# Performance work log

Measured on AMD Instinct MI355X. Metric: run time of the kernel, lower is better.

The kernel has to match this reference:

```python
import jax, jax.numpy as jnp
import numpy as np

C = 512
C8 = C // 8  # 64
B, H, W = 4, 64, 64


def setup_inputs() -> dict:
    key = jax.random.key(0)
    ks = jax.random.split(key, 8)
    s_in = 1.0 / np.sqrt(C)
    return {
        "x": jax.random.normal(ks[0], (B, C, H, W), dtype=jnp.float32),
        "Wf": jax.random.normal(ks[1], (C8, C), dtype=jnp.float32) * s_in,
        "bf": jax.random.normal(ks[2], (C8,), dtype=jnp.float32) * 0.01,
        "Wg": jax.random.normal(ks[3], (C8, C), dtype=jnp.float32) * s_in,
        "bg": jax.random.normal(ks[4], (C8,), dtype=jnp.float32) * 0.01,
        "Wh": jax.random.normal(ks[5], (C, C), dtype=jnp.float32) * s_in,
        "bh": jax.random.normal(ks[6], (C,), dtype=jnp.float32) * 0.01,
        # original inits gamma=0; use small nonzero so the attention path is exercised
        "gamma": jax.random.normal(ks[7], (1,), dtype=jnp.float32) * 0.1,
    }


def reference(x, Wf, bf, Wg, bg, Wh, bh, gamma):
    b, c, h, w = x.shape
    n = h * w
    xt = x.reshape(b, c, n)  # flatten spatial -> tokens (b, C, N)
    # 1x1 convs are per-token GEMMs
    f = jnp.einsum('bcn,oc->bno', xt, Wf) + bf          # (b, N, C8)
    g = jnp.einsum('bcn,oc->bon', xt, Wg) + bg[:, None]  # (b, C8, N)
    attn = jax.nn.softmax(jnp.einsum('bnk,bkm->bnm', f, g), axis=2)  # (b, N, N)
    hv = jnp.einsum('bcn,oc->bon', xt, Wh) + bh[:, None]  # (b, C, N)
    # torch.bmm(h, attention): out[:,c,j] = sum_i h[:,c,i] * attn[:,i,j]
    sa = jnp.einsum('bci,bij->bcj', hv, attn).reshape(b, c, h, w)
    return gamma[0] * sa + x
```

## Files before the change

kernel.cpp:

```cpp
#include <hip/hip_runtime.h>


#define Bq 4
#define Cq 512
#define Nq 4096
#define PSTR 72

typedef __attribute__((ext_vector_type(8))) short bf16x8;
typedef __attribute__((ext_vector_type(4))) float f32x4;

__device__ __forceinline__ short f2bf(float f) {
  unsigned u = __float_as_uint(f);
  u += 0x7fffu + ((u >> 16) & 1u);
  return (short)(u >> 16);
}
__device__ __forceinline__ float bf2f(short h) {
  return __uint_as_float(((unsigned)(unsigned short)h) << 16);
}

#define MFMA16(A, B, C) __builtin_amdgcn_mfma_f32_16x16x32_bf16((A), (B), (C), 0, 0, 0)

__device__ __forceinline__ size_t fg_frag(int b, int t16, int ss) {
  return ((size_t)((b * 256 + t16) * 2 + ss)) * 512;
}
__device__ __forceinline__ size_t hv_frag(int b, int tc, int si) {
  return ((size_t)((b * 32 + tc) * 128 + si)) * 512;
}

__global__ __launch_bounds__(256) void k_prepw(
    const float* __restrict__ Wf, const float* __restrict__ Wg,
    const float* __restrict__ Wh,
    short* __restrict__ whi, short* __restrict__ wlo, short* __restrict__ whb) {
  int gid = blockIdx.x * 256 + threadIdx.x;
  if (gid < 128 * 512) {
    int row = gid >> 9;
    float v = (row < 64) ? Wf[gid] : Wg[gid - 32768];
    short h = f2bf(v);
    whi[gid] = h;
    wlo[gid] = f2bf(v - bf2f(h));
  }
  whb[gid] = f2bf(Wh[gid]);
}

__global__ __launch_bounds__(256) void k_xpose(
    const float* __restrict__ x, short* __restrict__ xthi, short* __restrict__ xtlo) {
  int b = blockIdx.z, c0 = blockIdx.y * 64, n0 = blockIdx.x * 64;
  __shared__ float tile[64][65];
  int t = threadIdx.x;
  int l = t & 15, g = t >> 4;
  const float* xp = x + ((size_t)b * Cq + c0) * Nq + n0;
#pragma unroll
  for (int e = 0; e < 4; e++) {
    int cl = g + e * 16;
    float4 v = *(const float4*)(xp + (size_t)cl * Nq + l * 4);
    tile[cl][l * 4 + 0] = v.x; tile[cl][l * 4 + 1] = v.y;
    tile[cl][l * 4 + 2] = v.z; tile[cl][l * 4 + 3] = v.w;
  }
  __syncthreads();
#pragma unroll
  for (int e = 0; e < 4; e++) {
    int nl = g + e * 16;
    short hi[4], lo[4];
#pragma unroll
    for (int qq = 0; qq < 4; qq++) {
      float v = tile[l * 4 + qq][nl];
      hi[qq] = f2bf(v);
      lo[qq] = f2bf(v - bf2f(hi[qq]));
    }
    size_t off = ((size_t)b * Nq + n0 + nl) * Cq + c0 + l * 4;
    *(short4*)(xthi + off) = make_short4(hi[0], hi[1], hi[2], hi[3]);
    *(short4*)(xtlo + off) = make_short4(lo[0], lo[1], lo[2], lo[3]);
  }
}

__global__ __launch_bounds__(512) void k_fg(
    const short* __restrict__ xthi, const short* __restrict__ xtlo,
    const short* __restrict__ whi, const short* __restrict__ wlo,
    const float* __restrict__ bfv, const float* __restrict__ bgv,
    short* __restrict__ ffh, short* __restrict__ ffl,
    short* __restrict__ gfh, short* __restrict__ gfl) {
  int b = blockIdx.y, n0 = blockIdx.x * 64;
  int t = threadIdx.x, w = t >> 6, lane = t & 63, l15 = lane & 15, q = lane >> 4;
  int wr = w & 3, wh = w >> 2;
  const short* ah = xthi + ((size_t)b * Nq + n0 + wr * 16 + l15) * Cq;
  const short* al = xtlo + ((size_t)b * Nq + n0 + wr * 16 + l15) * Cq;
  f32x4 z = {0.f, 0.f, 0.f, 0.f};
  f32x4 acc[4] = {z, z, z, z};
  for (int ks = 0; ks < 16; ks++) {
    bf16x8 Ahi = *(const bf16x8*)(ah + ks * 32 + q * 8);
    bf16x8 Alo = *(const bf16x8*)(al + ks * 32 + q * 8);
#pragma unroll
    for (int os = 0; os < 4; os++) {
      int o = wh * 64 + os * 16 + l15;
      bf16x8 Bhi = *(const bf16x8*)(whi + o * 512 + ks * 32 + q * 8);
      bf16x8 Blo = *(const bf16x8*)(wlo + o * 512 + ks * 32 + q * 8);
      acc[os] = MFMA16(Alo, Bhi, acc[os]);
      acc[os] = MFMA16(Ahi, Blo, acc[os]);
      acc[os] = MFMA16(Ahi, Bhi, acc[os]);
    }
  }
#pragma unroll
  for (int os = 0; os < 4; os++) {
#pragma unroll
    for (int r = 0; r < 4; r++) {
      int o = os * 16 + l15;
      int n = n0 + wr * 16 + q * 4 + r;
      float v = acc[os][r] + (wh == 0 ? bfv[o] : bgv[o]);
      size_t off = ((size_t)((b * 256 + (n >> 4)) * 2 + (o >> 5))) * 512
                 + (((o >> 3) & 3) * 16 + (n & 15)) * 8 + (o & 7);
      short h = f2bf(v);
      short lo = f2bf(v - bf2f(h));
      if (wh == 0) { ffh[off] = h; ffl[off] = lo; }
      else         { gfh[off] = h; gfl[off] = lo; }
    }
  }
}

__global__ __launch_bounds__(512) void k_stats(
    const short* __restrict__ ffh, const short* __restrict__ ffl,
    const short* __restrict__ gfh, const short* __restrict__ gfl,
    float* __restrict__ lsum4) {
  int jch = blockIdx.x, jc = jch * 1024, i0 = blockIdx.y * 64, b = blockIdx.z;
  int t = threadIdx.x, w = t >> 6, lane = t & 63, l15 = lane & 15, q = lane >> 4;
  bf16x8 Ahi[4][2], Alo[4][2];
#pragma unroll
  for (int ig = 0; ig < 4; ig++)
#pragma unroll
    for (int ss = 0; ss < 2; ss++) {
      size_t base = fg_frag(b, (i0 >> 4) + ig, ss) + lane * 8;
      Ahi[ig][ss] = *(const bf16x8*)(ffh + base);
      Alo[ig][ss] = *(const bf16x8*)(ffl + base);
    }
  float ls[16];
#pragma unroll
  for (int a = 0; a < 16; a++) ls[a] = 0.f;
  f32x4 z = {0.f, 0.f, 0.f, 0.f};
  for (int jt = 0; jt < 8; jt++) {
    int tj = (jc >> 4) + w * 8 + jt;
    bf16x8 GBh[2], GBl[2];
#pragma unroll
    for (int ss = 0; ss < 2; ss++) {
      size_t base = fg_frag(b, tj, ss) + lane * 8;
      GBh[ss] = *(const bf16x8*)(gfh + base);
      GBl[ss] = *(const bf16x8*)(gfl + base);
    }
#pragma unroll
    for (int ig = 0; ig < 4; ig++) {
      f32x4 sh = z, sl = z;
#pragma unroll
      for (int ss = 0; ss < 2; ss++) {
        sl = MFMA16(Alo[ig][ss], GBh[ss], sl);
        sl = MFMA16(Ahi[ig][ss], GBl[ss], sl);
        sh = MFMA16(Ahi[ig][ss], GBh[ss], sh);
      }
#pragma unroll
      for (int r = 0; r < 4; r++) ls[ig * 4 + r] += __expf(sh[r] + sl[r]);
    }
  }
#pragma unroll
  for (int m = 1; m < 16; m <<= 1) {
#pragma unroll
    for (int a = 0; a < 16; a++) ls[a] += __shfl_xor(ls[a], m, 64);
  }
  __shared__ float part[8][64];
  if (l15 == 0) {
#pragma unroll
    for (int ig = 0; ig < 4; ig++)
#pragma unroll
      for (int r = 0; r < 4; r++) part[w][ig * 16 + q * 4 + r] = ls[ig * 4 + r];
  }
  __syncthreads();
  if (t < 64) {
    float s = 0.f;
#pragma unroll
    for (int ww = 0; ww < 8; ww++) s += part[ww][t];
    lsum4[(size_t)jch * 16384 + (size_t)b * Nq + i0 + t] = s;
  }
}

__global__ __launch_bounds__(512) void k_hv(
    const short* __restrict__ whb, const short* __restrict__ xthi,
    const float* __restrict__ bhv, const float* __restrict__ lsum4,
    short* __restrict__ hvf) {
  int si = blockIdx.x, b = blockIdx.y;
  int t = threadIdx.x, w = t >> 6, lane = t & 63, l15 = lane & 15, q = lane >> 4;
  int c0 = w * 64;
  const short* ar0 = xthi + ((size_t)b * Nq + si * 32 + l15) * Cq;
  const short* ar1 = ar0 + 16 * Cq;
  f32x4 z = {0.f, 0.f, 0.f, 0.f};
  f32x4 acc[2][4];
#pragma unroll
  for (int a = 0; a < 2; a++)
#pragma unroll
    for (int c = 0; c < 4; c++) acc[a][c] = z;
  for (int ks = 0; ks < 16; ks++) {
    bf16x8 A0 = *(const bf16x8*)(ar0 + ks * 32 + q * 8);
    bf16x8 A1 = *(const bf16x8*)(ar1 + ks * 32 + q * 8);
#pragma unroll
    for (int ct = 0; ct < 4; ct++) {
      bf16x8 Bv = *(const bf16x8*)(whb + (size_t)(c0 + ct * 16 + l15) * 512 + ks * 32 + q * 8);
      acc[0][ct] = MFMA16(A0, Bv, acc[0][ct]);
      acc[1][ct] = MFMA16(A1, Bv, acc[1][ct]);
    }
  }
  float li[2][4];
#pragma unroll
  for (int it = 0; it < 2; it++)
#pragma unroll
    for (int r = 0; r < 4; r++) {
      size_t idx = (size_t)b * Nq + si * 32 + it * 16 + q * 4 + r;
      float s = lsum4[idx] + lsum4[16384 + idx] + lsum4[32768 + idx] + lsum4[49152 + idx];
      li[it][r] = 1.0f / s;
    }
  int src0 = ((q & 1) << 5) + l15;
  int src1 = src0 + 16;
  int hiSel = q >> 1;
#pragma unroll
  for (int ct = 0; ct < 4; ct++) {
    float bias = bhv[c0 + ct * 16 + l15];
    unsigned u01[2], u23[2];
#pragma unroll
    for (int it = 0; it < 2; it++) {
      float v0 = (acc[it][ct][0] + bias) * li[it][0];
      float v1 = (acc[it][ct][1] + bias) * li[it][1];
      float v2 = (acc[it][ct][2] + bias) * li[it][2];
      float v3 = (acc[it][ct][3] + bias) * li[it][3];
      u01[it] = (unsigned)(unsigned short)f2bf(v0) | ((unsigned)(unsigned short)f2bf(v1) << 16);
      u23[it] = (unsigned)(unsigned short)f2bf(v2) | ((unsigned)(unsigned short)f2bf(v3) << 16);
    }
    unsigned a0 = __shfl((int)u01[0], src0), b0 = __shfl((int)u01[1], src0);
    unsigned a1 = __shfl((int)u23[0], src0), b1 = __shfl((int)u23[1], src0);
    unsigned a2 = __shfl((int)u01[0], src1), b2 = __shfl((int)u01[1], src1);
    unsigned a3 = __shfl((int)u23[0], src1), b3 = __shfl((int)u23[1], src1);
    uint4 st;
    st.x = hiSel ? b0 : a0;
    st.y = hiSel ? b1 : a1;
    st.z = hiSel ? b2 : a2;
    st.w = hiSel ? b3 : a3;
    *(uint4*)(hvf + hv_frag(b, (c0 >> 4) + ct, si) + (size_t)lane * 8) = st;
  }
}

__global__ __launch_bounds__(1024, 4) void k_attn(
    const short* __restrict__ ffh, const short* __restrict__ ffl,
    const short* __restrict__ gfh, const short* __restrict__ gfl,
    const short* __restrict__ hvf, const float* __restrict__ x,
    const float* __restrict__ gp, float* __restrict__ out) {
  int L = blockIdx.x;
  int b = (L & 7) >> 1;
  int jt64 = ((L >> 3) << 1) | (L & 1);
  int j0 = jt64 * 64;
  int t = threadIdx.x, w = t >> 6, lane = t & 63, l15 = lane & 15, q = lane >> 4;
  int iq = w & 3, jh = w >> 2;
  int cg = w & 7, jg = w >> 3;
  __shared__ __align__(16) short pt[2][64 * PSTR];
  float gamma = gp[0];
  f32x4 z = {0.f, 0.f, 0.f, 0.f};
  f32x4 acc[4][2];
#pragma unroll
  for (int a = 0; a < 4; a++)
#pragma unroll
    for (int bb = 0; bb < 2; bb++) acc[a][bb] = z;
  bf16x8 GBh[2], GBl[2];
#pragma unroll
  for (int ss = 0; ss < 2; ss++) {
    size_t base = fg_frag(b, (j0 >> 4) + jh, ss) + lane * 8;
    GBh[ss] = *(const bf16x8*)(gfh + base);
    GBl[ss] = *(const bf16x8*)(gfl + base);
  }

  auto computeS = [&](int it, int buf) {
    bf16x8 Ah[2], Al[2];
#pragma unroll
    for (int ss = 0; ss < 2; ss++) {
      size_t base = fg_frag(b, it * 4 + iq, ss) + lane * 8;
      Ah[ss] = *(const bf16x8*)(ffh + base);
      Al[ss] = *(const bf16x8*)(ffl + base);
    }
    f32x4 sh = z, sl = z;
#pragma unroll
    for (int ss = 0; ss < 2; ss++) {
      sl = MFMA16(Al[ss], GBh[ss], sl);
      sl = MFMA16(Ah[ss], GBl[ss], sl);
      sh = MFMA16(Ah[ss], GBh[ss], sh);
    }
    unsigned p01 = (unsigned)(unsigned short)f2bf(__expf(sh[0] + sl[0])) |
                   ((unsigned)(unsigned short)f2bf(__expf(sh[1] + sl[1])) << 16);
    unsigned p23 = (unsigned)(unsigned short)f2bf(__expf(sh[2] + sl[2])) |
                   ((unsigned)(unsigned short)f2bf(__expf(sh[3] + sl[3])) << 16);
    uint2 pv; pv.x = p01; pv.y = p23;
    *(uint2*)(&pt[buf][(jh * 16 + l15) * PSTR + iq * 16 + q * 4]) = pv;
  };

  computeS(0, 0);
  for (int it = 0; it < 64; it++) {
    __syncthreads();
    int buf = it & 1;
    if (it < 63) computeS(it + 1, 1 - buf);
#pragma unroll
    for (int ss = 0; ss < 2; ss++) {
      bf16x8 PB[2];
#pragma unroll
      for (int jt = 0; jt < 2; jt++)
        PB[jt] = *(const bf16x8*)(&pt[buf][(jg * 32 + jt * 16 + l15) * PSTR + ss * 32 + q * 8]);
#pragma unroll
      for (int ct = 0; ct < 4; ct++) {
        size_t hb = hv_frag(b, cg * 4 + ct, it * 2 + ss) + lane * 8;
        bf16x8 A = *(const bf16x8*)(hvf + hb);
#pragma unroll
        for (int jt = 0; jt < 2; jt++)
          acc[ct][jt] = MFMA16(A, PB[jt], acc[ct][jt]);
      }
    }
  }
#pragma unroll
  for (int ct = 0; ct < 4; ct++) {
#pragma unroll
    for (int jt = 0; jt < 2; jt++) {
#pragma unroll
      for (int r = 0; r < 4; r++) {
        int c = cg * 64 + ct * 16 + q * 4 + r;
        int j = j0 + jg * 32 + jt * 16 + l15;
        size_t off = ((size_t)b * Cq + c) * Nq + j;
        out[off] = gamma * acc[ct][jt][r] + x[off];
      }
    }
  }
}

extern "C" void kernel_launch(void* const* d_in, const int* in_sizes, int n_in,
                              void* d_out, int out_size, void* d_ws, size_t ws_size,
                              hipStream_t stream) {
  (void)in_sizes; (void)n_in; (void)out_size; (void)ws_size;
  const float* x  = (const float*)d_in[0];
  const float* Wf = (const float*)d_in[1];
  const float* bf = (const float*)d_in[2];
  const float* Wg = (const float*)d_in[3];
  const float* bg = (const float*)d_in[4];
  const float* Wh = (const float*)d_in[5];
  const float* bh = (const float*)d_in[6];
  const float* gm = (const float*)d_in[7];
  float* out = (float*)d_out;
  char* ws = (char*)d_ws;
  short* xthi  = (short*)(ws);
  short* xtlo  = (short*)(ws + 16777216);
  short* ffh   = (short*)(ws + 33554432);
  short* ffl   = (short*)(ws + 35651584);
  short* gfh   = (short*)(ws + 37748736);
  short* gfl   = (short*)(ws + 39845888);
  short* whi   = (short*)(ws + 41943040);
  short* wlo   = (short*)(ws + 42074112);
  short* whb   = (short*)(ws + 42205184);
  float* lsum4 = (float*)(ws + 42729472);
  short* hvf   = (short*)(ws + 42991616);

  hipLaunchKernelGGL(k_prepw, dim3(1024), dim3(256), 0, stream, Wf, Wg, Wh, whi, wlo, whb);
  hipLaunchKernelGGL(k_xpose, dim3(64, 8, 4), dim3(256), 0, stream, x, xthi, xtlo);
  hipLaunchKernelGGL(k_fg, dim3(64, 4), dim3(512), 0, stream,
                     xthi, xtlo, whi, wlo, bf, bg, ffh, ffl, gfh, gfl);
  hipLaunchKernelGGL(k_stats, dim3(4, 64, 4), dim3(512), 0, stream, ffh, ffl, gfh, gfl, lsum4);
  hipLaunchKernelGGL(k_hv, dim3(128, 4), dim3(512), 0, stream, whb, xthi, bh, lsum4, hvf);
  hipLaunchKernelGGL(k_attn, dim3(256), dim3(1024), 0, stream,
                     ffh, ffl, gfh, gfl, hvf, x, gm, out);
}
```

Measured before the change: 359.7 us.

## Materialize exp(S) in stats kernel and replace attention with streaming PV GEMM

k_stats now writes the bf16 exponentiated scores into a large global P buffer in MFMA fragment layout while accumulating row sums. The attention kernel becomes k_pv, which loads hv and P fragments straight from global memory and runs only the PV MFMAs, with no score recomputation or LDS staging. This trades the recompute of scores and the barriers for roughly 128 MB of extra global writes and repeated reads of P.

```diff
diff --git a/kernel.cpp b/kernel.cpp
--- a/kernel.cpp
+++ b/kernel.cpp
@@ -4,7 +4,6 @@
 #define Bq 4
 #define Cq 512
 #define Nq 4096
-#define PSTR 72
 
 typedef __attribute__((ext_vector_type(8))) short bf16x8;
 typedef __attribute__((ext_vector_type(4))) float f32x4;
@@ -25,6 +24,9 @@
 }
 __device__ __forceinline__ size_t hv_frag(int b, int tc, int si) {
   return ((size_t)((b * 32 + tc) * 128 + si)) * 512;
+}
+__device__ __forceinline__ size_t p_frag(int b, int jt16, int si) {
+  return ((size_t)((b * 256 + jt16) * 128 + si)) * 512;
 }
 
 __global__ __launch_bounds__(256) void k_prepw(
@@ -119,7 +121,7 @@
 __global__ __launch_bounds__(512) void k_stats(
     const short* __restrict__ ffh, const short* __restrict__ ffl,
     const short* __restrict__ gfh, const short* __restrict__ gfl,
-    float* __restrict__ lsum4) {
+    float* __restrict__ lsum4, short* __restrict__ pmat) {
   int jch = blockIdx.x, jc = jch * 1024, i0 = blockIdx.y * 64, b = blockIdx.z;
   int t = threadIdx.x, w = t >> 6, lane = t & 63, l15 = lane & 15, q = lane >> 4;
   bf16x8 Ahi[4][2], Alo[4][2];
@@ -153,8 +155,20 @@
         sl = MFMA16(Ahi[ig][ss], GBl[ss], sl);
         sh = MFMA16(Ahi[ig][ss], GBh[ss], sh);
       }
-#pragma unroll
-      for (int r = 0; r < 4; r++) ls[ig * 4 + r] += __expf(sh[r] + sl[r]);
+      float ev[4];
+#pragma unroll
+      for (int r = 0; r < 4; r++) {
+        ev[r] = __expf(sh[r] + sl[r]);
+        ls[ig * 4 + r] += ev[r];
+      }
+      uint2 pv;
+      pv.x = (unsigned)(unsigned short)f2bf(ev[0]) |
+             ((unsigned)(unsigned short)f2bf(ev[1]) << 16);
+      pv.y = (unsigned)(unsigned short)f2bf(ev[2]) |
+             ((unsigned)(unsigned short)f2bf(ev[3]) << 16);
+      size_t pb = p_frag(b, tj, (i0 >> 5) + (ig >> 1)) +
+                  (size_t)(((ig & 1) * 2 + (q >> 1)) * 128 + l15 * 8 + (q & 1) * 4);
+      *(uint2*)(pmat + pb) = pv;
     }
   }
 #pragma unroll
@@ -241,19 +255,17 @@
   }
 }
 
-__global__ __launch_bounds__(1024, 4) void k_attn(
-    const short* __restrict__ ffh, const short* __restrict__ ffl,
-    const short* __restrict__ gfh, const short* __restrict__ gfl,
-    const short* __restrict__ hvf, const float* __restrict__ x,
-    const float* __restrict__ gp, float* __restrict__ out) {
+__global__ __launch_bounds__(512, 4) void k_pv(
+    const short* __restrict__ hvf, const short* __restrict__ pmat,
+    const float* __restrict__ x, const float* __restrict__ gp,
+    float* __restrict__ out) {
   int L = blockIdx.x;
-  int b = (L & 7) >> 1;
-  int jt64 = ((L >> 3) << 1) | (L & 1);
+  int combo = L & 7;
+  int b = combo >> 1, ch = combo & 1;
+  int jt64 = L >> 3;
   int j0 = jt64 * 64;
   int t = threadIdx.x, w = t >> 6, lane = t & 63, l15 = lane & 15, q = lane >> 4;
-  int iq = w & 3, jh = w >> 2;
-  int cg = w & 7, jg = w >> 3;
-  __shared__ __align__(16) short pt[2][64 * PSTR];
+  int cg = w & 3, jg = w >> 2;
   float gamma = gp[0];
   f32x4 z = {0.f, 0.f, 0.f, 0.f};
   f32x4 acc[4][2];
@@ -261,57 +273,24 @@
   for (int a = 0; a < 4; a++)
 #pragma unroll
     for (int bb = 0; bb < 2; bb++) acc[a][bb] = z;
-  bf16x8 GBh[2], GBl[2];
-#pragma unroll
-  for (int ss = 0; ss < 2; ss++) {
-    size_t base = fg_frag(b, (j0 >> 4) + jh, ss) + lane * 8;
-    GBh[ss] = *(const bf16x8*)(gfh + base);
-    GBl[ss] = *(const bf16x8*)(gfl + base);
-  }
-
-  auto computeS = [&](int it, int buf) {
-    bf16x8 Ah[2], Al[2];
-#pragma unroll
-    for (int ss = 0; ss < 2; ss++) {
-      size_t base = fg_frag(b, it * 4 + iq, ss) + lane * 8;
-      Ah[ss] = *(const bf16x8*)(ffh + base);
-      Al[ss] = *(const bf16x8*)(ffl + base);
-    }
-    f32x4 sh = z, sl = z;
-#pragma unroll
-    for (int ss = 0; ss < 2; ss++) {
-      sl = MFMA16(Al[ss], GBh[ss], sl);
-      sl = MFMA16(Ah[ss], GBl[ss], sl);
-      sh = MFMA16(Ah[ss], GBh[ss], sh);
-    }
-    unsigned p01 = (unsigned)(unsigned short)f2bf(__expf(sh[0] + sl[0])) |
-                   ((unsigned)(unsigned short)f2bf(__expf(sh[1] + sl[1])) << 16);
-    unsigned p23 = (unsigned)(unsigned short)f2bf(__expf(sh[2] + sl[2])) |
-                   ((unsigned)(unsigned short)f2bf(__expf(sh[3] + sl[3])) << 16);
-    uint2 pv; pv.x = p01; pv.y = p23;
-    *(uint2*)(&pt[buf][(jh * 16 + l15) * PSTR + iq * 16 + q * 4]) = pv;
-  };
-
-  computeS(0, 0);
-  for (int it = 0; it < 64; it++) {
-    __syncthreads();
-    int buf = it & 1;
-    if (it < 63) computeS(it + 1, 1 - buf);
-#pragma unroll
-    for (int ss = 0; ss < 2; ss++) {
-      bf16x8 PB[2];
+  const short* hbase = hvf + (size_t)lane * 8;
+  const short* pbase = pmat + (size_t)lane * 8;
+  int tc0 = ch * 16 + cg * 4;
+  int jp0 = (j0 >> 4) + jg * 2;
+#pragma unroll 2
+  for (int si = 0; si < 128; si++) {
+    bf16x8 HV[4], PB[2];
+#pragma unroll
+    for (int ct = 0; ct < 4; ct++)
+      HV[ct] = *(const bf16x8*)(hbase + hv_frag(b, tc0 + ct, si));
+#pragma unroll
+    for (int jt = 0; jt < 2; jt++)
+      PB[jt] = *(const bf16x8*)(pbase + p_frag(b, jp0 + jt, si));
+#pragma unroll
+    for (int ct = 0; ct < 4; ct++)
 #pragma unroll
       for (int jt = 0; jt < 2; jt++)
-        PB[jt] = *(const bf16x8*)(&pt[buf][(jg * 32 + jt * 16 + l15) * PSTR + ss * 32 + q * 8]);
-#pragma unroll
-      for (int ct = 0; ct < 4; ct++) {
-        size_t hb = hv_frag(b, cg * 4 + ct, it * 2 + ss) + lane * 8;
-        bf16x8 A = *(const bf16x8*)(hvf + hb);
-#pragma unroll
-        for (int jt = 0; jt < 2; jt++)
-          acc[ct][jt] = MFMA16(A, PB[jt], acc[ct][jt]);
-      }
-    }
+        acc[ct][jt] = MFMA16(HV[ct], PB[jt], acc[ct][jt]);
   }
 #pragma unroll
   for (int ct = 0; ct < 4; ct++) {
@@ -319,7 +298,7 @@
     for (int jt = 0; jt < 2; jt++) {
 #pragma unroll
       for (int r = 0; r < 4; r++) {
-        int c = cg * 64 + ct * 16 + q * 4 + r;
+        int c = ch * 256 + cg * 64 + ct * 16 + q * 4 + r;
         int j = j0 + jg * 32 + jt * 16 + l15;
         size_t off = ((size_t)b * Cq + c) * Nq + j;
         out[off] = gamma * acc[ct][jt][r] + x[off];
@@ -353,13 +332,14 @@
   short* whb   = (short*)(ws + 42205184);
   float* lsum4 = (float*)(ws + 42729472);
   short* hvf   = (short*)(ws + 42991616);
+  short* pmat  = (short*)(ws + 59768832);
 
   hipLaunchKernelGGL(k_prepw, dim3(1024), dim3(256), 0, stream, Wf, Wg, Wh, whi, wlo, whb);
   hipLaunchKernelGGL(k_xpose, dim3(64, 8, 4), dim3(256), 0, stream, x, xthi, xtlo);
   hipLaunchKernelGGL(k_fg, dim3(64, 4), dim3(512), 0, stream,
                      xthi, xtlo, whi, wlo, bf, bg, ffh, ffl, gfh, gfl);
-  hipLaunchKernelGGL(k_stats, dim3(4, 64, 4), dim3(512), 0, stream, ffh, ffl, gfh, gfl, lsum4);
+  hipLaunchKernelGGL(k_stats, dim3(4, 64, 4), dim3(512), 0, stream,
+                     ffh, ffl, gfh, gfl, lsum4, pmat);
   hipLaunchKernelGGL(k_hv, dim3(128, 4), dim3(512), 0, stream, whb, xthi, bh, lsum4, hvf);
-  hipLaunchKernelGGL(k_attn, dim3(256), dim3(1024), 0, stream,
-                     ffh, ffl, gfh, gfl, hvf, x, gm, out);
-}
+  hipLaunchKernelGGL(k_pv, dim3(512), dim3(512), 0, stream, hvf, pmat, x, gm, out);
+}
```

Measured after the change: 325.8 us. 9.4% less time.
